# Kernel optimization log

Measured on AMD Instinct MI355X. Metric: run time of the kernel, lower is better.

## Reference

```python
import jax, jax.numpy as jnp
import numpy as np

B, S, D, H, E, K, V, FF, P = 1, 2048, 1024, 16, 8, 2, 32000, 4096, 4096
HD = D // H
EPS = 1e-5


def setup_inputs() -> dict:
    key = jax.random.key(0)
    ks = iter(jax.random.split(key, 64))
    w = lambda shape: jax.random.normal(next(ks), shape, jnp.float32) * 0.02
    d = {}
    d['input_ids'] = jax.random.randint(next(ks), (B, S), 0, V)
    d['embed_w'] = w((V, D))
    d['pos_w'] = w((P, D))
    for i in (0, 1):
        d[f'b{i}_ln1_g'] = jnp.ones(D); d[f'b{i}_ln1_b'] = jnp.zeros(D)
        d[f'b{i}_in_w'] = w((3 * D, D)); d[f'b{i}_in_b'] = jnp.zeros(3 * D)
        d[f'b{i}_out_w'] = w((D, D)); d[f'b{i}_out_b'] = jnp.zeros(D)
        d[f'b{i}_ln2_g'] = jnp.ones(D); d[f'b{i}_ln2_b'] = jnp.zeros(D)
    d['b0_ffn_w1'] = w((FF, D)); d['b0_ffn_b1'] = jnp.zeros(FF)
    d['b0_ffn_w2'] = w((D, FF)); d['b0_ffn_b2'] = jnp.zeros(D)
    d['b1_gate_w'] = w((E, D)); d['b1_gate_b'] = jnp.zeros(E)
    d['b1_moe_w1'] = w((E, FF, D)); d['b1_moe_b1'] = jnp.zeros((E, FF))
    d['b1_moe_w2'] = w((E, D, FF)); d['b1_moe_b2'] = jnp.zeros((E, D))
    d['norm_g'] = jnp.ones(D); d['norm_b'] = jnp.zeros(D)
    d['head_w'] = w((V, D))
    return d


def _ln(x, g, b):
    m = jnp.mean(x, -1, keepdims=True)
    v = jnp.mean(jnp.square(x - m), -1, keepdims=True)
    return (x - m) * jax.lax.rsqrt(v + EPS) * g + b


def _mha(x, in_w, in_b, out_w, out_b):
    # torch nn.MultiheadAttention (batch_first, eval mode -> no dropout)
    qkv = x @ in_w.T + in_b  # [B,S,3D]
    q, k, v = jnp.split(qkv, 3, axis=-1)
    q = q.reshape(B, S, H, HD); k = k.reshape(B, S, H, HD); v = v.reshape(B, S, H, HD)
    scores = jnp.einsum('bqhd,bkhd->bhqk', q, k) / jnp.sqrt(jnp.float32(HD))
    attn = jax.nn.softmax(scores, axis=-1)
    o = jnp.einsum('bhqk,bkhd->bqhd', attn, v).reshape(B, S, D)
    return o @ out_w.T + out_b


def _moe(h, gate_w, gate_b, w1, b1, w2, b2):
    scores = h @ gate_w.T + gate_b                       # [B,S,E]
    top_s, top_i = jax.lax.top_k(scores, K)              # [B,S,K]
    weights = jax.nn.softmax(top_s, axis=-1)             # softmax over top-k
    onehot = jax.nn.one_hot(top_i, E, dtype=h.dtype)     # [B,S,K,E]
    combine = jnp.sum(onehot * weights[..., None], axis=-2)  # [B,S,E]
    hid = jax.nn.gelu(jnp.einsum('bsd,efd->bsef', h, w1) + b1, approximate=False)
    eo = jnp.einsum('bsef,edf->bsed', hid, w2) + b2      # [B,S,E,D]
    return jnp.einsum('bsed,bse->bsd', eo, combine)


def reference(input_ids, embed_w, pos_w,
              b0_ln1_g, b0_ln1_b, b0_in_w, b0_in_b, b0_out_w, b0_out_b, b0_ln2_g, b0_ln2_b,
              b0_ffn_w1, b0_ffn_b1, b0_ffn_w2, b0_ffn_b2,
              b1_ln1_g, b1_ln1_b, b1_in_w, b1_in_b, b1_out_w, b1_out_b, b1_ln2_g, b1_ln2_b,
              b1_gate_w, b1_gate_b, b1_moe_w1, b1_moe_b1, b1_moe_w2, b1_moe_b2,
              norm_g, norm_b, head_w):
    pos = jnp.arange(S)[None, :]
    x = jnp.take(embed_w, input_ids, axis=0) + jnp.take(pos_w, pos, axis=0)
    # block 0: dense FFN
    x = x + _mha(_ln(x, b0_ln1_g, b0_ln1_b), b0_in_w, b0_in_b, b0_out_w, b0_out_b)
    h = _ln(x, b0_ln2_g, b0_ln2_b)
    ffn = jax.nn.gelu(h @ b0_ffn_w1.T + b0_ffn_b1, approximate=False) @ b0_ffn_w2.T + b0_ffn_b2
    x = x + ffn  # integration layer assumed residual add
    # block 1: MoE
    x = x + _mha(_ln(x, b1_ln1_g, b1_ln1_b), b1_in_w, b1_in_b, b1_out_w, b1_out_b)
    h = _ln(x, b1_ln2_g, b1_ln2_b)
    x = x + _moe(h, b1_gate_w, b1_gate_b, b1_moe_w1, b1_moe_b1, b1_moe_w2, b1_moe_b2)
    x = _ln(x, norm_g, norm_b)
    return x @ head_w.T
```

## Files before the change

### kernel.cpp

```cpp
#include <hip/hip_runtime.h>
#include <hip/hip_bf16.h>
#include <math.h>

typedef unsigned short ushort_t;
typedef __attribute__((ext_vector_type(8))) __bf16 bf16x8;
typedef __attribute__((ext_vector_type(4))) float f32x4;
typedef __attribute__((ext_vector_type(8))) short s8v;
typedef __attribute__((ext_vector_type(4))) short s4v;

#define SQ 2048
#define DM 1024
#define NH 16
#define HDIM 64
#define FFD 4096
#define NVOC 32000

__device__ inline float b2f(unsigned short u) {
  union { unsigned int i; float f; } x; x.i = ((unsigned int)u) << 16; return x.f;
}
__device__ inline unsigned short f2b(float f) {
  __hip_bfloat16 h = __float2bfloat16(f);
  return *reinterpret_cast<unsigned short*>(&h);
}
__device__ inline void split2(float x, ushort_t& h, ushort_t& l) {
  h = f2b(x);
  l = f2b(x - b2f(h));
}
__device__ inline float geluf(float v) {
  return 0.5f * v * (1.0f + erff(v * 0.70710678118654752f));
}
__device__ __forceinline__ void gld16(const void* g, void* l) {
  __builtin_amdgcn_global_load_lds(
      (const __attribute__((address_space(1))) void*)g,
      (__attribute__((address_space(3))) void*)l, 16, 0, 0);
}
#define MFMA __builtin_amdgcn_mfma_f32_16x16x32_bf16

template<int EPI, int NT, int KS>
__device__ __forceinline__ void gemmsp_body(
    const ushort_t* __restrict__ AH, const ushort_t* __restrict__ AL,
    int lda, long long bA,
    const ushort_t* __restrict__ BH, const ushort_t* __restrict__ BL,
    int ldb, long long bB,
    float* __restrict__ C, ushort_t* __restrict__ CH, ushort_t* __restrict__ CL,
    int ldc, long long bC, long long pC,
    int M, int N, int K, const float* __restrict__ bias, float alpha,
    ushort_t* __restrict__ TH, ushort_t* __restrict__ TL)
{
  int z = blockIdx.z, h = z / KS, kc = z % KS;
  const ushort_t* AHp = AH + (long long)h * bA + (long long)kc * K;
  const ushort_t* ALp = AL + (long long)h * bA + (long long)kc * K;
  const ushort_t* BHp = BH + (long long)h * bB + (long long)kc * K;
  const ushort_t* BLp = BL + (long long)h * bB + (long long)kc * K;
  int m0 = blockIdx.x * 128, n0 = blockIdx.y * NT;
  const int NF = NT / 32;

  __shared__ __align__(16) ushort_t sAH[128 * 32], sAL[128 * 32];
  __shared__ __align__(16) ushort_t sBH[NT * 32],  sBL[NT * 32];

  int tid = threadIdx.x, lane = tid & 63, wave = tid >> 6;
  int wr = (wave >> 1) * 64, wc = (wave & 1) * (NT >> 1);
  int l15 = lane & 15, l4 = lane >> 4;

  f32x4 acc[4][NF];
#pragma unroll
  for (int m = 0; m < 4; ++m)
#pragma unroll
    for (int n = 0; n < NF; ++n) acc[m][n] = (f32x4){0.f, 0.f, 0.f, 0.f};

  for (int k0 = 0; k0 < K; k0 += 32) {
#pragma unroll
    for (int i = 0; i < 2; ++i) {
      int fi = i * 2048 + tid * 8;
      int r = fi >> 5, chk = (fi >> 3) & 3;
      int scol = ((chk ^ ((r >> 1) & 3)) << 3);
      int ra = m0 + r; if (ra > M - 1) ra = M - 1;
      long long go = (long long)ra * lda + k0 + scol;
      gld16(AHp + go, &sAH[fi]);
      gld16(ALp + go, &sAL[fi]);
    }
#pragma unroll
    for (int i = 0; i < NT / 64; ++i) {
      int fi = i * 2048 + tid * 8;
      int r = fi >> 5, chk = (fi >> 3) & 3;
      int scol = ((chk ^ ((r >> 1) & 3)) << 3);
      int rb = n0 + r; if (rb > N - 1) rb = N - 1;
      long long go = (long long)rb * ldb + k0 + scol;
      gld16(BHp + go, &sBH[fi]);
      gld16(BLp + go, &sBL[fi]);
    }
    __syncthreads();
    bf16x8 ah[4], al[4], bh[NF], bl[NF];
#pragma unroll
    for (int m = 0; m < 4; ++m) {
      int r = wr + m * 16 + l15;
      int o = r * 32 + ((l4 ^ ((r >> 1) & 3)) << 3);
      ah[m] = *(const bf16x8*)&sAH[o];
      al[m] = *(const bf16x8*)&sAL[o];
    }
#pragma unroll
    for (int n = 0; n < NF; ++n) {
      int r = wc + n * 16 + l15;
      int o = r * 32 + ((l4 ^ ((r >> 1) & 3)) << 3);
      bh[n] = *(const bf16x8*)&sBH[o];
      bl[n] = *(const bf16x8*)&sBL[o];
    }
#pragma unroll
    for (int m = 0; m < 4; ++m)
#pragma unroll
      for (int n = 0; n < NF; ++n) {
        acc[m][n] = MFMA(ah[m], bh[n], acc[m][n], 0, 0, 0);
        acc[m][n] = MFMA(al[m], bh[n], acc[m][n], 0, 0, 0);
        acc[m][n] = MFMA(ah[m], bl[n], acc[m][n], 0, 0, 0);
      }
    __syncthreads();
  }

  if (EPI == 5 && n0 >= 2 * DM) {
#pragma unroll
    for (int m = 0; m < 4; ++m) {
      int rbase = m0 + wr + m * 16 + l4 * 4;
#pragma unroll
      for (int n = 0; n < NF; ++n) {
        int c = n0 + wc + n * 16 + l15;
        int d = c - 2 * DM;
        float bv = bias[c];
        s4v hv, lv;
#pragma unroll
        for (int q = 0; q < 4; ++q) {
          ushort_t hh, ll; split2(acc[m][n][q] + bv, hh, ll);
          hv[q] = (short)hh; lv[q] = (short)ll;
        }
        *(s4v*)&TH[(long long)d * SQ + rbase] = hv;
        *(s4v*)&TL[(long long)d * SQ + rbase] = lv;
      }
    }
    return;
  }

#pragma unroll
  for (int m = 0; m < 4; ++m) {
#pragma unroll
    for (int n = 0; n < NF; ++n) {
      int c = n0 + wc + n * 16 + l15;
      if (c >= N) continue;
      float bv = (EPI == 4 || EPI == 5) ? bias[c] : 0.f;
#pragma unroll
      for (int q = 0; q < 4; ++q) {
        int rr = m0 + wr + m * 16 + l4 * 4 + q;
        if (rr >= M) continue;
        float v = acc[m][n][q];
        if (EPI == 5) {
          ushort_t hh, ll; split2(v + bv, hh, ll);
          long long o = (long long)rr * ldc + c; CH[o] = hh; CL[o] = ll;
        } else if (EPI == 2) {
          C[(long long)kc * pC + (long long)rr * ldc + (long long)h * bC + c] = v;
        } else if (EPI == 4) {
          ushort_t hh, ll; split2(geluf(v + bv), hh, ll);
          long long o = (long long)rr * ldc + c; CH[o] = hh; CL[o] = ll;
        }
      }
    }
  }
}

#define SP_ARGS const ushort_t* AH, const ushort_t* AL, int lda, long long bA, \
    const ushort_t* BH, const ushort_t* BL, int ldb, long long bB, \
    float* C, ushort_t* CH, ushort_t* CL, int ldc, long long bC, long long pC, \
    int M, int N, int K, const float* bias, float alpha, \
    ushort_t* TH, ushort_t* TL
#define SP_PASS AH, AL, lda, bA, BH, BL, ldb, bB, C, CH, CL, ldc, bC, pC, M, N, K, bias, alpha, TH, TL

__global__ __launch_bounds__(256) void k_qkv (SP_ARGS) { gemmsp_body<5,128,1>(SP_PASS); }
__global__ __launch_bounds__(256) void k_outp(SP_ARGS) { gemmsp_body<2, 64,4>(SP_PASS); }
__global__ __launch_bounds__(256) void k_ffn1(SP_ARGS) { gemmsp_body<4,128,1>(SP_PASS); }
__global__ __launch_bounds__(256) void k_ffn2(SP_ARGS) { gemmsp_body<2, 64,2>(SP_PASS); }

__global__ __launch_bounds__(256)
void k_attn(const ushort_t* __restrict__ qkvH, const ushort_t* __restrict__ qkvL,
            const ushort_t* __restrict__ VtH, const ushort_t* __restrict__ VtL,
            ushort_t* __restrict__ aH, ushort_t* __restrict__ aL)
{
  int f = blockIdx.x + blockIdx.y * gridDim.x;
  int logical = (f & 7) * 64 + (f >> 3);
  int q0 = (logical & 31) * 64;
  int h  = logical >> 5;

  __shared__ __align__(16) ushort_t sKH[4096], sKL[4096];
  __shared__ __align__(16) ushort_t sVH[4096], sVL[4096];
  __shared__ __align__(16) ushort_t sPH[4096], sPL[4096];

  int tid = threadIdx.x, lane = tid & 63, wave = tid >> 6;
  int l15 = lane & 15, l4 = lane >> 4;

  bf16x8 qh[2], ql[2];
  {
    long long base = (long long)(q0 + wave * 16 + l15) * (3 * DM) + h * 64 + l4 * 8;
    qh[0] = *(const bf16x8*)(qkvH + base);
    qh[1] = *(const bf16x8*)(qkvH + base + 32);
    ql[0] = *(const bf16x8*)(qkvL + base);
    ql[1] = *(const bf16x8*)(qkvL + base + 32);
  }

  float mrow[4], lrow[4];
  f32x4 Oacc[4];
#pragma unroll
  for (int r = 0; r < 4; ++r) { mrow[r] = -1e30f; lrow[r] = 0.f; }
#pragma unroll
  for (int n = 0; n < 4; ++n) Oacc[n] = (f32x4){0.f, 0.f, 0.f, 0.f};

  for (int kt = 0; kt < SQ / 64; ++kt) {
#pragma unroll
    for (int i = 0; i < 2; ++i) {
      int idx = i * 2048 + tid * 8;
      int row = idx >> 6, chk = (idx >> 3) & 7;
      int scol = ((chk ^ (row & 7)) << 3);
      long long gk = (long long)(kt * 64 + row) * (3 * DM) + DM + h * 64 + scol;
      long long gv = (long long)(h * 64 + row) * SQ + kt * 64 + scol;
      gld16(qkvH + gk, &sKH[idx]);
      gld16(qkvL + gk, &sKL[idx]);
      gld16(VtH + gv, &sVH[idx]);
      gld16(VtL + gv, &sVL[idx]);
    }
    __syncthreads();

    f32x4 S[4];
#pragma unroll
    for (int n = 0; n < 4; ++n) S[n] = (f32x4){0.f, 0.f, 0.f, 0.f};
#pragma unroll
    for (int kk = 0; kk < 64; kk += 32) {
      int kkI = kk >> 5;
      bf16x8 qhf = qh[kkI], qlf = ql[kkI];
#pragma unroll
      for (int n = 0; n < 4; ++n) {
        int br = n * 16 + l15;
        int bo = br * 64 + ((((kk >> 3) + l4) ^ (br & 7)) << 3);
        bf16x8 kh = *(const bf16x8*)&sKH[bo];
        bf16x8 kl = *(const bf16x8*)&sKL[bo];
        S[n] = MFMA(qhf, kh, S[n], 0, 0, 0);
        S[n] = MFMA(qlf, kh, S[n], 0, 0, 0);
        S[n] = MFMA(qhf, kl, S[n], 0, 0, 0);
      }
    }
    float tm[4], ts[4];
#pragma unroll
    for (int r = 0; r < 4; ++r) {
#pragma unroll
      for (int n = 0; n < 4; ++n) S[n][r] *= 0.125f;
      tm[r] = fmaxf(fmaxf(S[0][r], S[1][r]), fmaxf(S[2][r], S[3][r]));
    }
#pragma unroll
    for (int mk = 1; mk <= 8; mk <<= 1)
#pragma unroll
      for (int r = 0; r < 4; ++r) tm[r] = fmaxf(tm[r], __shfl_xor(tm[r], mk));
#pragma unroll
    for (int r = 0; r < 4; ++r) {
      float mn = fmaxf(mrow[r], tm[r]);
      float corr = __expf(mrow[r] - mn);
      mrow[r] = mn;
      float s = 0.f;
#pragma unroll
      for (int n = 0; n < 4; ++n) { S[n][r] = __expf(S[n][r] - mn); s += S[n][r]; }
      ts[r] = s;
      lrow[r] *= corr;
#pragma unroll
      for (int n = 0; n < 4; ++n) Oacc[n][r] *= corr;
    }
#pragma unroll
    for (int mk = 1; mk <= 8; mk <<= 1)
#pragma unroll
      for (int r = 0; r < 4; ++r) ts[r] += __shfl_xor(ts[r], mk);
#pragma unroll
    for (int r = 0; r < 4; ++r) lrow[r] += ts[r];

    {
      ushort_t* pH = &sPH[wave * 1024];
      ushort_t* pL = &sPL[wave * 1024];
#pragma unroll
      for (int n = 0; n < 4; ++n)
#pragma unroll
        for (int r = 0; r < 4; ++r) {
          int row = l4 * 4 + r, col = n * 16 + l15;
          int ad = row * 64 + (((col >> 3) ^ (row & 7)) << 3) + (col & 7);
          ushort_t hh, ll; split2(S[n][r], hh, ll);
          pH[ad] = hh; pL[ad] = ll;
        }
    }
    __syncthreads();
#pragma unroll
    for (int kk = 0; kk < 64; kk += 32) {
      int ao = wave * 1024 + l15 * 64 + ((((kk >> 3) + l4) ^ (l15 & 7)) << 3);
      bf16x8 ph = *(const bf16x8*)&sPH[ao];
      bf16x8 pl = *(const bf16x8*)&sPL[ao];
#pragma unroll
      for (int n = 0; n < 4; ++n) {
        int br = n * 16 + l15;
        int bo = br * 64 + ((((kk >> 3) + l4) ^ (br & 7)) << 3);
        bf16x8 vh = *(const bf16x8*)&sVH[bo];
        bf16x8 vl = *(const bf16x8*)&sVL[bo];
        Oacc[n] = MFMA(ph, vh, Oacc[n], 0, 0, 0);
        Oacc[n] = MFMA(pl, vh, Oacc[n], 0, 0, 0);
        Oacc[n] = MFMA(ph, vl, Oacc[n], 0, 0, 0);
      }
    }
    __syncthreads();
  }

#pragma unroll
  for (int n = 0; n < 4; ++n)
#pragma unroll
    for (int r = 0; r < 4; ++r) {
      int q = q0 + wave * 16 + l4 * 4 + r;
      int d = h * 64 + n * 16 + l15;
      float val = Oacc[n][r] / lrow[r];
      ushort_t hh, ll; split2(val, hh, ll);
      long long o = (long long)q * DM + d;
      aH[o] = hh; aL[o] = ll;
    }
}

template<int EPI, int BSRC, int SWAP, int KS, int XS>
__device__ __forceinline__ void gemm16_body(
    const ushort_t* __restrict__ A, int lda, long long bA,
    const void* __restrict__ Bv, int ldb, long long bB,
    void* __restrict__ Cv, int ldc, long long bC, long long pC,
    int M, int N, int K, const float* __restrict__ bias, int bBias,
    const int* __restrict__ offs)
{
  int bz = blockIdx.z;
  int z = bz / KS, kc = bz % KS;
  int Kc = K / KS;
  const ushort_t* Ap = A + (long long)z * bA + (long long)kc * Kc;
  int rowStart = 0, Meff = M;
  if (offs) { rowStart = offs[z]; Meff = offs[z + 1] - rowStart; }
  int bx = blockIdx.x, by = blockIdx.y;
  if (XS) {
    int flat = bx + by * gridDim.x;
    int cpx = (gridDim.x * gridDim.y) >> 3;
    int s = (flat & 7) * cpx + (flat >> 3);
    bx = s % gridDim.x; by = s / gridDim.x;
  }
  int m0 = (SWAP ? by : bx) * 128;
  if (m0 >= Meff) return;
  int n0 = (SWAP ? bx : by) * 128;

  __shared__ __align__(16) char smem[32768];
  ushort_t* As = (ushort_t*)smem;
  ushort_t* Bs = (ushort_t*)(smem + 16384);

  int tid = threadIdx.x, lane = tid & 63, wave = tid >> 6;
  int wr = (wave >> 1) * 64, wc = (wave & 1) * 64;
  int l15 = lane & 15, l4 = lane >> 4;

  f32x4 acc[4][4];
#pragma unroll
  for (int m = 0; m < 4; ++m)
#pragma unroll
    for (int n = 0; n < 4; ++n) acc[m][n] = (f32x4){0.f, 0.f, 0.f, 0.f};

  for (int k0 = 0; k0 < Kc; k0 += 64) {
#pragma unroll
    for (int i = 0; i < 4; ++i) {
      int idx = i * 2048 + tid * 8;
      int row = idx >> 6, chk = (idx >> 3) & 7;
      int scol = ((chk ^ (row & 7)) << 3);
      int ra = m0 + row; if (ra > Meff - 1) ra = Meff - 1;
      gld16(Ap + (long long)(rowStart + ra) * lda + k0 + scol, &As[idx]);
    }
    if (BSRC == 1) {
      const ushort_t* Bp = (const ushort_t*)Bv + (long long)z * bB + (long long)kc * Kc;
#pragma unroll
      for (int i = 0; i < 4; ++i) {
        int idx = i * 2048 + tid * 8;
        int row = idx >> 6, chk = (idx >> 3) & 7;
        int scol = ((chk ^ (row & 7)) << 3);
        int rb = n0 + row; if (rb > N - 1) rb = N - 1;
        gld16(Bp + (long long)rb * ldb + k0 + scol, &Bs[idx]);
      }
    } else {
      const float* Bf = (const float*)Bv + (long long)z * bB + (long long)kc * Kc;
#pragma unroll
      for (int i = 0; i < 8; ++i) {
        int g = tid + i * 256;
        int r = g >> 4, c4 = (g & 15) * 4;
        int rb = n0 + r; if (rb > N - 1) rb = N - 1;
        float4 fv = *(const float4*)(Bf + (long long)rb * ldb + k0 + c4);
        s4v o; o[0] = (short)f2b(fv.x); o[1] = (short)f2b(fv.y);
        o[2] = (short)f2b(fv.z); o[3] = (short)f2b(fv.w);
        int dst = r * 64 + (((c4 >> 3) ^ (r & 7)) << 3) + (c4 & 7);
        *(s4v*)&Bs[dst] = o;
      }
    }
    __syncthreads();
#pragma unroll
    for (int kk = 0; kk < 64; kk += 32) {
      bf16x8 af[4], bfr[4];
#pragma unroll
      for (int m = 0; m < 4; ++m) {
        int r = wr + m * 16 + l15;
        af[m] = *(const bf16x8*)&As[r * 64 + ((((kk >> 3) + l4) ^ (r & 7)) << 3)];
      }
#pragma unroll
      for (int n = 0; n < 4; ++n) {
        int r = wc + n * 16 + l15;
        bfr[n] = *(const bf16x8*)&Bs[r * 64 + ((((kk >> 3) + l4) ^ (r & 7)) << 3)];
      }
#pragma unroll
      for (int m = 0; m < 4; ++m)
#pragma unroll
        for (int n = 0; n < 4; ++n)
          acc[m][n] = MFMA(af[m], bfr[n], acc[m][n], 0, 0, 0);
    }
    __syncthreads();
  }

  if (EPI == 6 || EPI == 7) {
    float* fE = (float*)smem;
#pragma unroll
    for (int h2 = 0; h2 < 2; ++h2) {
      if ((wave >> 1) == h2) {
#pragma unroll
        for (int m = 0; m < 4; ++m)
#pragma unroll
          for (int n = 0; n < 4; ++n)
#pragma unroll
            for (int q = 0; q < 4; ++q)
              fE[(m * 16 + l4 * 4 + q) * 128 + wc + n * 16 + l15] = acc[m][n][q];
      }
      __syncthreads();
#pragma unroll
      for (int i = 0; i < 8; ++i) {
        int lin = tid + i * 256;
        int row = lin >> 5, c4 = (lin & 31) << 2;
        int gr = m0 + h2 * 64 + row;
        if (gr < Meff) {
          f32x4 v4 = *(const f32x4*)&fE[row * 128 + c4];
          long long crow = rowStart + gr;
          float* dst = (float*)Cv + (EPI == 7 ? (long long)kc * pC : 0LL)
                       + crow * ldc + n0 + c4;
          if (EPI == 6) __builtin_nontemporal_store(v4, (f32x4*)dst);
          else          *(f32x4*)dst = v4;
        }
      }
      __syncthreads();
    }
    return;
  }

#pragma unroll
  for (int m = 0; m < 4; ++m) {
#pragma unroll
    for (int n = 0; n < 4; ++n) {
      int c = n0 + wc + n * 16 + l15;
      if (c >= N) continue;
      float bv = (EPI == 2) ? bias[(long long)z * bBias + c] : 0.f;
#pragma unroll
      for (int q = 0; q < 4; ++q) {
        int rr = m0 + wr + m * 16 + l4 * 4 + q;
        if (rr >= Meff) continue;
        float v = acc[m][n][q];
        long long crow = rowStart + rr;
        if (EPI == 2)
          ((ushort_t*)Cv)[crow * ldc + (long long)z * bC + c] = f2b(geluf(v + bv));
      }
    }
  }
}

#define G16_ARGS const ushort_t* A, int lda, long long bA, const void* Bv, \
    int ldb, long long bB, void* Cv, int ldc, long long bC, long long pC, \
    int M, int N, int K, const float* bias, int bBias, const int* offs
#define G16_PASS A, lda, bA, Bv, ldb, bB, Cv, ldc, bC, pC, M, N, K, bias, bBias, offs

__global__ __launch_bounds__(256) void k_moe1   (G16_ARGS) { gemm16_body<2,1,1,1,0>(G16_PASS); }
__global__ __launch_bounds__(256) void k_moe2   (G16_ARGS) { gemm16_body<7,1,1,2,0>(G16_PASS); }
__global__ __launch_bounds__(256) void k_head_bf(G16_ARGS) { gemm16_body<6,1,0,1,1>(G16_PASS); }
__global__ __launch_bounds__(256) void k_head_f (G16_ARGS) { gemm16_body<6,0,0,1,1>(G16_PASS); }

__global__ __launch_bounds__(256)
void cvt_split2(const float* __restrict__ s0, ushort_t* __restrict__ dh0,
                ushort_t* __restrict__ dl0,
                const float* __restrict__ s1, ushort_t* __restrict__ dh1,
                ushort_t* __restrict__ dl1, int n4)
{
  const float* s = blockIdx.y ? s1 : s0;
  ushort_t* dh = blockIdx.y ? dh1 : dh0;
  ushort_t* dl = blockIdx.y ? dl1 : dl0;
  int i = blockIdx.x * blockDim.x + threadIdx.x;
  int stride = gridDim.x * blockDim.x;
  for (; i < n4; i += stride) {
    float4 f = ((const float4*)s)[i];
    s4v h, l; ushort_t hh, ll;
    split2(f.x, hh, ll); h[0] = (short)hh; l[0] = (short)ll;
    split2(f.y, hh, ll); h[1] = (short)hh; l[1] = (short)ll;
    split2(f.z, hh, ll); h[2] = (short)hh; l[2] = (short)ll;
    split2(f.w, hh, ll); h[3] = (short)hh; l[3] = (short)ll;
    ((s4v*)dh)[i] = h; ((s4v*)dl)[i] = l;
  }
}

__global__ __launch_bounds__(256)
void cvt_bf16(const float* __restrict__ s, ushort_t* __restrict__ d, int n4)
{
  int i = blockIdx.x * blockDim.x + threadIdx.x;
  int stride = gridDim.x * blockDim.x;
  for (; i < n4; i += stride) {
    float4 f = ((const float4*)s)[i];
    s4v o; o[0] = (short)f2b(f.x); o[1] = (short)f2b(f.y);
    o[2] = (short)f2b(f.z); o[3] = (short)f2b(f.w);
    ((s4v*)d)[i] = o;
  }
}

__global__ __launch_bounds__(256)
void embed_kernel(const int* __restrict__ ids, const float* __restrict__ ew,
                  const float* __restrict__ pw, float* __restrict__ x,
                  int* __restrict__ counts)
{
  int srow = blockIdx.x, tid = threadIdx.x;
  if (srow == 0 && tid < 8) counts[tid] = 0;
  int id = ids[srow];
  const float4 e = *(const float4*)(ew + (long long)id * DM + tid * 4);
  const float4 p = *(const float4*)(pw + (long long)srow * DM + tid * 4);
  float4* xr = (float4*)(x + (long long)srow * DM) + tid;
  *xr = make_float4(e.x + p.x, e.y + p.y, e.z + p.z, e.w + p.w);
}

template<int MODE, int NP>
__global__ __launch_bounds__(256)
void ln_fused(float* __restrict__ x, const float* __restrict__ P, long long pC,
              const float* __restrict__ bias_pre,
              const float* __restrict__ g, const float* __restrict__ b,
              ushort_t* __restrict__ outH, ushort_t* __restrict__ outL)
{
  int row = blockIdx.x, tid = threadIdx.x;
  long long xo = (long long)row * DM + tid * 4;
  float4 v = *(const float4*)(x + xo);
  if (NP > 0) {
    float4 bp = *(const float4*)(bias_pre + tid * 4);
    float sx = bp.x, sy = bp.y, sz = bp.z, sw = bp.w;
#pragma unroll
    for (int p = 0; p < NP; ++p) {
      float4 pv = *(const float4*)(P + (long long)p * pC + xo);
      sx += pv.x; sy += pv.y; sz += pv.z; sw += pv.w;
    }
    v.x += sx; v.y += sy; v.z += sz; v.w += sw;
    *(float4*)(x + xo) = v;
  }
  __shared__ float sm1[4], sm2[4];
  float s = v.x + v.y + v.z + v.w;
  for (int o = 32; o > 0; o >>= 1) s += __shfl_down(s, o);
  if ((tid & 63) == 0) sm1[tid >> 6] = s;
  __syncthreads();
  float mean = (sm1[0] + sm1[1] + sm1[2] + sm1[3]) * (1.0f / DM);
  float d0 = v.x - mean, d1 = v.y - mean, d2 = v.z - mean, d3 = v.w - mean;
  float q = d0 * d0 + d1 * d1 + d2 * d2 + d3 * d3;
  for (int o = 32; o > 0; o >>= 1) q += __shfl_down(q, o);
  if ((tid & 63) == 0) sm2[tid >> 6] = q;
  __syncthreads();
  float var = (sm2[0] + sm2[1] + sm2[2] + sm2[3]) * (1.0f / DM);
  float rstd = rsqrtf(var + 1e-5f);
  float4 gv = ((const float4*)g)[tid];
  float4 bv = ((const float4*)b)[tid];
  float o0 = d0 * rstd * gv.x + bv.x, o1 = d1 * rstd * gv.y + bv.y;
  float o2 = d2 * rstd * gv.z + bv.z, o3 = d3 * rstd * gv.w + bv.w;
  long long base = (long long)row * DM + tid * 4;
  if (MODE == 0) {
    ushort_t hh, ll;
    split2(o0, hh, ll); outH[base + 0] = hh; outL[base + 0] = ll;
    split2(o1, hh, ll); outH[base + 1] = hh; outL[base + 1] = ll;
    split2(o2, hh, ll); outH[base + 2] = hh; outL[base + 2] = ll;
    split2(o3, hh, ll); outH[base + 3] = hh; outL[base + 3] = ll;
  } else {
    outH[base + 0] = f2b(o0); outH[base + 1] = f2b(o1);
    outH[base + 2] = f2b(o2); outH[base + 3] = f2b(o3);
  }
}

__global__ __launch_bounds__(256)
void ln_gate_top2(float* __restrict__ x, const float* __restrict__ P,
                  long long pC, const float* __restrict__ bias_pre,
                  const float* __restrict__ g, const float* __restrict__ b,
                  const float* __restrict__ gw, const float* __restrict__ gb,
                  int* __restrict__ topi, float* __restrict__ topw,
                  int* __restrict__ counts, ushort_t* __restrict__ outH)
{
  int row = blockIdx.x, tid = threadIdx.x;
  long long xo = (long long)row * DM + tid * 4;
  float4 v = *(const float4*)(x + xo);
  {
    float4 bp = *(const float4*)(bias_pre + tid * 4);
    float sx = bp.x, sy = bp.y, sz = bp.z, sw = bp.w;
#pragma unroll
    for (int p = 0; p < 4; ++p) {
      float4 pv = *(const float4*)(P + (long long)p * pC + xo);
      sx += pv.x; sy += pv.y; sz += pv.z; sw += pv.w;
    }
    v.x += sx; v.y += sy; v.z += sz; v.w += sw;
    *(float4*)(x + xo) = v;
  }
  __shared__ float sm1[4], sm2[4];
  __shared__ float se[8][4];
  float s = v.x + v.y + v.z + v.w;
  for (int o = 32; o > 0; o >>= 1) s += __shfl_down(s, o);
  if ((tid & 63) == 0) sm1[tid >> 6] = s;
  __syncthreads();
  float mean = (sm1[0] + sm1[1] + sm1[2] + sm1[3]) * (1.0f / DM);
  float d0 = v.x - mean, d1 = v.y - mean, d2 = v.z - mean, d3 = v.w - mean;
  float q = d0 * d0 + d1 * d1 + d2 * d2 + d3 * d3;
  for (int o = 32; o > 0; o >>= 1) q += __shfl_down(q, o);
  if ((tid & 63) == 0) sm2[tid >> 6] = q;
  __syncthreads();
  float var = (sm2[0] + sm2[1] + sm2[2] + sm2[3]) * (1.0f / DM);
  float rstd = rsqrtf(var + 1e-5f);
  float4 gv = ((const float4*)g)[tid];
  float4 bv = ((const float4*)b)[tid];
  float h0 = d0 * rstd * gv.x + bv.x, h1 = d1 * rstd * gv.y + bv.y;
  float h2 = d2 * rstd * gv.z + bv.z, h3 = d3 * rstd * gv.w + bv.w;
  long long base = (long long)row * DM + tid * 4;
  outH[base + 0] = f2b(h0); outH[base + 1] = f2b(h1);
  outH[base + 2] = f2b(h2); outH[base + 3] = f2b(h3);
#pragma unroll
  for (int e = 0; e < 8; ++e) {
    float4 w = ((const float4*)(gw + (long long)e * DM))[tid];
    float p = h0 * w.x + h1 * w.y + h2 * w.z + h3 * w.w;
    for (int o = 32; o > 0; o >>= 1) p += __shfl_down(p, o);
    if ((tid & 63) == 0) se[e][tid >> 6] = p;
  }
  __syncthreads();
  if (tid == 0) {
    float sc[8];
#pragma unroll
    for (int e = 0; e < 8; ++e)
      sc[e] = se[e][0] + se[e][1] + se[e][2] + se[e][3] + gb[e];
    int i1 = 0; float m1 = sc[0];
    for (int e = 1; e < 8; ++e) if (sc[e] > m1) { m1 = sc[e]; i1 = e; }
    int i2 = -1; float m2 = -1e30f;
    for (int e = 0; e < 8; ++e) if (e != i1 && sc[e] > m2) { m2 = sc[e]; i2 = e; }
    float e2 = __expf(m2 - m1);
    float w1 = 1.f / (1.f + e2);
    topi[row * 2] = i1; topi[row * 2 + 1] = i2;
    topw[row * 2] = w1; topw[row * 2 + 1] = 1.f - w1;
    atomicAdd(&counts[i1], 1);
    atomicAdd(&counts[i2], 1);
  }
}

__global__ void moe_prefix(const int* __restrict__ counts, int* __restrict__ offs,
                           int* __restrict__ cursors)
{
  if (threadIdx.x == 0 && blockIdx.x == 0) {
    int a = 0;
    for (int e = 0; e < 8; ++e) { offs[e] = a; a += counts[e]; cursors[e] = 0; }
    offs[8] = a;
  }
}

__global__ __launch_bounds__(256)
void moe_gather(const ushort_t* __restrict__ hH, const int* __restrict__ topi,
                const float* __restrict__ topw, const int* __restrict__ offs,
                int* __restrict__ cursors, int* __restrict__ tokIdx,
                float* __restrict__ tokW, int* __restrict__ slotOf,
                ushort_t* __restrict__ Xg)
{
  int tok = blockIdx.x, tid = threadIdx.x;
  __shared__ int s0s, s1s;
  if (tid == 0) {
    int e0 = topi[tok * 2], e1 = topi[tok * 2 + 1];
    int s0 = offs[e0] + atomicAdd(&cursors[e0], 1);
    int s1 = offs[e1] + atomicAdd(&cursors[e1], 1);
    tokIdx[s0] = tok; tokW[s0] = topw[tok * 2];
    tokIdx[s1] = tok; tokW[s1] = topw[tok * 2 + 1];
    slotOf[tok * 2] = s0; slotOf[tok * 2 + 1] = s1;
    s0s = s0; s1s = s1;
  }
  __syncthreads();
  s4v v = ((const s4v*)(hH + (long long)tok * DM))[tid];
  ((s4v*)(Xg + (long long)s0s * DM))[tid] = v;
  ((s4v*)(Xg + (long long)s1s * DM))[tid] = v;
}

__global__ __launch_bounds__(256)
void moe_ln_final(const float* __restrict__ x, const float* __restrict__ eo,
                  long long pC, const int* __restrict__ slotOf,
                  const int* __restrict__ topi, const float* __restrict__ topw,
                  const float* __restrict__ b2, const float* __restrict__ g,
                  const float* __restrict__ b, ushort_t* __restrict__ outH)
{
  int tok = blockIdx.x, tid = threadIdx.x;
  int s0 = slotOf[tok * 2], s1 = slotOf[tok * 2 + 1];
  int e0 = topi[tok * 2], e1 = topi[tok * 2 + 1];
  float w0 = topw[tok * 2], w1 = topw[tok * 2 + 1];
  float4 a  = ((const float4*)(eo + (long long)s0 * DM))[tid];
  float4 a2 = ((const float4*)(eo + pC + (long long)s0 * DM))[tid];
  float4 bb1= ((const float4*)(eo + (long long)s1 * DM))[tid];
  float4 bb2= ((const float4*)(eo + pC + (long long)s1 * DM))[tid];
  float4 ba = ((const float4*)(b2 + (long long)e0 * DM))[tid];
  float4 bbb= ((const float4*)(b2 + (long long)e1 * DM))[tid];
  float4 v = ((const float4*)(x + (long long)tok * DM))[tid];
  v.x += w0 * (a.x + a2.x + ba.x) + w1 * (bb1.x + bb2.x + bbb.x);
  v.y += w0 * (a.y + a2.y + ba.y) + w1 * (bb1.y + bb2.y + bbb.y);
  v.z += w0 * (a.z + a2.z + ba.z) + w1 * (bb1.z + bb2.z + bbb.z);
  v.w += w0 * (a.w + a2.w + ba.w) + w1 * (bb1.w + bb2.w + bbb.w);
  __shared__ float sm1[4], sm2[4];
  float s = v.x + v.y + v.z + v.w;
  for (int o = 32; o > 0; o >>= 1) s += __shfl_down(s, o);
  if ((tid & 63) == 0) sm1[tid >> 6] = s;
  __syncthreads();
  float mean = (sm1[0] + sm1[1] + sm1[2] + sm1[3]) * (1.0f / DM);
  float d0 = v.x - mean, d1 = v.y - mean, d2 = v.z - mean, d3 = v.w - mean;
  float q = d0 * d0 + d1 * d1 + d2 * d2 + d3 * d3;
  for (int o = 32; o > 0; o >>= 1) q += __shfl_down(q, o);
  if ((tid & 63) == 0) sm2[tid >> 6] = q;
  __syncthreads();
  float var = (sm2[0] + sm2[1] + sm2[2] + sm2[3]) * (1.0f / DM);
  float rstd = rsqrtf(var + 1e-5f);
  float4 gv = ((const float4*)g)[tid];
  float4 bv = ((const float4*)b)[tid];
  long long base = (long long)tok * DM + tid * 4;
  outH[base + 0] = f2b(d0 * rstd * gv.x + bv.x);
  outH[base + 1] = f2b(d1 * rstd * gv.y + bv.y);
  outH[base + 2] = f2b(d2 * rstd * gv.z + bv.z);
  outH[base + 3] = f2b(d3 * rstd * gv.w + bv.w);
}

extern "C" void kernel_launch(void* const* d_in, const int* in_sizes, int n_in,
                              void* d_out, int out_size, void* d_ws, size_t ws_size,
                              hipStream_t stream)
{
  const int* ids = (const int*)d_in[0];
  const float* embed_w = (const float*)d_in[1];
  const float* pos_w   = (const float*)d_in[2];
  const float* ln1_g[2] = {(const float*)d_in[3],  (const float*)d_in[11]};
  const float* ln1_b[2] = {(const float*)d_in[4],  (const float*)d_in[12]};
  const float* in_w[2]  = {(const float*)d_in[5],  (const float*)d_in[13]};
  const float* in_b[2]  = {(const float*)d_in[6],  (const float*)d_in[14]};
  const float* out_w[2] = {(const float*)d_in[7],  (const float*)d_in[15]};
  const float* out_b[2] = {(const float*)d_in[8],  (const float*)d_in[16]};
  const float* ln2_g[2] = {(const float*)d_in[9],  (const float*)d_in[17]};
  const float* ln2_b[2] = {(const float*)d_in[10], (const float*)d_in[18]};
  const float* ffn_w1 = (const float*)d_in[19];
  const float* ffn_b1 = (const float*)d_in[20];
  const float* ffn_w2 = (const float*)d_in[21];
  const float* ffn_b2 = (const float*)d_in[22];
  const float* gate_w = (const float*)d_in[23];
  const float* gate_b = (const float*)d_in[24];
  const float* moe_w1 = (const float*)d_in[25];
  const float* moe_b1 = (const float*)d_in[26];
  const float* moe_w2 = (const float*)d_in[27];
  const float* moe_b2 = (const float*)d_in[28];
  const float* norm_g = (const float*)d_in[29];
  const float* norm_b = (const float*)d_in[30];
  const float* head_w = (const float*)d_in[31];

  char* ob = (char*)d_out;
  size_t off = 0;
  auto alloc = [&](size_t bytes) {
    char* p = ob + off;
    off = (off + bytes + 255) & ~(size_t)255;
    return p;
  };
  float*    x      = (float*)alloc((size_t)SQ * DM * 4);
  ushort_t* hbufH  = (ushort_t*)alloc((size_t)SQ * DM * 2);
  ushort_t* hbufL  = (ushort_t*)alloc((size_t)SQ * DM * 2);
  ushort_t* qkvH   = (ushort_t*)alloc((size_t)SQ * 3 * DM * 2);
  ushort_t* qkvL   = (ushort_t*)alloc((size_t)SQ * 3 * DM * 2);
  ushort_t* VtH    = (ushort_t*)alloc((size_t)NH * HDIM * SQ * 2);
  ushort_t* VtL    = (ushort_t*)alloc((size_t)NH * HDIM * SQ * 2);
  char*     resv   = (char*)alloc((size_t)32 << 20);
  ushort_t* attnH  = (ushort_t*)alloc((size_t)SQ * DM * 2);
  ushort_t* attnL  = (ushort_t*)alloc((size_t)SQ * DM * 2);
  ushort_t* Xg     = (ushort_t*)alloc((size_t)2 * SQ * DM * 2);
  int*      topi   = (int*)alloc(SQ * 2 * 4);
  float*    topw   = (float*)alloc(SQ * 2 * 4);
  int*      tokIdx = (int*)alloc(2 * SQ * 4);
  float*    tokW   = (float*)alloc(2 * SQ * 4);
  int*      slotOf = (int*)alloc(2 * SQ * 4);
  int*      counts = (int*)alloc(256);
  int*      offsb  = (int*)alloc(256);
  int*      cursors= (int*)alloc(256);
  ushort_t* ffnH   = (ushort_t*)alloc((size_t)SQ * FFD * 2);
  ushort_t* ffnL   = (ushort_t*)alloc((size_t)SQ * FFD * 2);
  float*    eo     = (float*)alloc((size_t)2 * 2 * SQ * DM * 4);
  ushort_t* inwH[2], *inwL[2], *outwH[2], *outwL[2];
  ushort_t* wsplit0 = (ushort_t*)alloc(0);
  inwH[0]  = (ushort_t*)alloc((size_t)3 * DM * DM * 2);
  inwL[0]  = (ushort_t*)alloc((size_t)3 * DM * DM * 2);
  inwH[1]  = (ushort_t*)alloc((size_t)3 * DM * DM * 2);
  inwL[1]  = (ushort_t*)alloc((size_t)3 * DM * DM * 2);
  outwH[0] = (ushort_t*)alloc((size_t)DM * DM * 2);
  outwL[0] = (ushort_t*)alloc((size_t)DM * DM * 2);
  outwH[1] = (ushort_t*)alloc((size_t)DM * DM * 2);
  outwL[1] = (ushort_t*)alloc((size_t)DM * DM * 2);
  ushort_t* f1H = (ushort_t*)alloc((size_t)FFD * DM * 2);
  ushort_t* f1L = (ushort_t*)alloc((size_t)FFD * DM * 2);
  ushort_t* f2H = (ushort_t*)alloc((size_t)DM * FFD * 2);
  ushort_t* f2L = (ushort_t*)alloc((size_t)DM * FFD * 2);
  ushort_t* moe_w1b = wsplit0;
  ushort_t* moe_w2b = qkvH;
  ushort_t* moehid  = ffnH;
  float*    pp      = eo;
  const long long eoPC = (long long)2 * SQ * DM;
  const long long ppPC = (long long)SQ * DM;
  ushort_t* hfin    = (ushort_t*)d_ws;
  bool wsBig = ws_size >= ((size_t)70 << 20);
  ushort_t* head_wb = (ushort_t*)((char*)d_ws + ((size_t)4 << 20));
  (void)resv;

  embed_kernel<<<SQ, 256, 0, stream>>>(ids, embed_w, pos_w, x, counts);
  cvt_split2<<<dim3(512, 2), 256, 0, stream>>>(
      in_w[0], inwH[0], inwL[0], in_w[1], inwH[1], inwL[1], 3 * DM * DM / 4);
  cvt_split2<<<dim3(512, 2), 256, 0, stream>>>(
      out_w[0], outwH[0], outwL[0], out_w[1], outwH[1], outwL[1], DM * DM / 4);
  cvt_split2<<<dim3(512, 2), 256, 0, stream>>>(
      ffn_w1, f1H, f1L, ffn_w2, f2H, f2L, FFD * DM / 4);
  if (wsBig)
    cvt_bf16<<<1024, 256, 0, stream>>>(head_w, head_wb, NVOC * DM / 4);

  ln_fused<0, 0><<<SQ, 256, 0, stream>>>(x, nullptr, 0, nullptr,
                                         ln1_g[0], ln1_b[0], hbufH, hbufL);
  k_qkv<<<dim3(16, 24, 1), 256, 0, stream>>>(
      hbufH, hbufL, DM, 0, inwH[0], inwL[0], DM, 0,
      nullptr, qkvH, qkvL, 3 * DM, 0, 0,
      SQ, 3 * DM, DM, in_b[0], 1.f, VtH, VtL);
  k_attn<<<dim3(SQ / 64, NH), 256, 0, stream>>>(qkvH, qkvL, VtH, VtL,
                                                attnH, attnL);
  k_outp<<<dim3(16, 16, 4), 256, 0, stream>>>(
      attnH, attnL, DM, 0, outwH[0], outwL[0], DM, 0,
      pp, nullptr, nullptr, DM, 0, ppPC,
      SQ, DM, DM / 4, nullptr, 1.f, nullptr, nullptr);
  ln_fused<0, 4><<<SQ, 256, 0, stream>>>(x, pp, ppPC, out_b[0],
                                         ln2_g[0], ln2_b[0], hbufH, hbufL);
  k_ffn1<<<dim3(16, 32, 1), 256, 0, stream>>>(
      hbufH, hbufL, DM, 0, f1H, f1L, DM, 0,
      nullptr, ffnH, ffnL, FFD, 0, 0,
      SQ, FFD, DM, ffn_b1, 1.f, nullptr, nullptr);
  k_ffn2<<<dim3(16, 16, 2), 256, 0, stream>>>(
      ffnH, ffnL, FFD, 0, f2H, f2L, FFD, 0,
      pp, nullptr, nullptr, DM, 0, ppPC,
      SQ, DM, FFD / 2, nullptr, 1.f, nullptr, nullptr);
  ln_fused<0, 2><<<SQ, 256, 0, stream>>>(x, pp, ppPC, ffn_b2,
                                         ln1_g[1], ln1_b[1], hbufH, hbufL);
  k_qkv<<<dim3(16, 24, 1), 256, 0, stream>>>(
      hbufH, hbufL, DM, 0, inwH[1], inwL[1], DM, 0,
      nullptr, qkvH, qkvL, 3 * DM, 0, 0,
      SQ, 3 * DM, DM, in_b[1], 1.f, VtH, VtL);
  k_attn<<<dim3(SQ / 64, NH), 256, 0, stream>>>(qkvH, qkvL, VtH, VtL,
                                                attnH, attnL);
  k_outp<<<dim3(16, 16, 4), 256, 0, stream>>>(
      attnH, attnL, DM, 0, outwH[1], outwL[1], DM, 0,
      pp, nullptr, nullptr, DM, 0, ppPC,
      SQ, DM, DM / 4, nullptr, 1.f, nullptr, nullptr);
  cvt_bf16<<<2048, 256, 0, stream>>>(moe_w1, moe_w1b, 8 * FFD * DM / 4);
  cvt_bf16<<<2048, 256, 0, stream>>>(moe_w2, moe_w2b, 8 * DM * FFD / 4);
  ln_gate_top2<<<SQ, 256, 0, stream>>>(x, pp, ppPC, out_b[1],
                                       ln2_g[1], ln2_b[1], gate_w, gate_b,
                                       topi, topw, counts, hbufH);
  moe_prefix<<<1, 64, 0, stream>>>(counts, offsb, cursors);
  moe_gather<<<SQ, 256, 0, stream>>>(hbufH, topi, topw, offsb, cursors,
                                     tokIdx, tokW, slotOf, Xg);
  k_moe1<<<dim3(32, 16, 8), 256, 0, stream>>>(
      Xg, DM, 0, moe_w1b, DM, (long long)FFD * DM,
      moehid, FFD, 0, 0, SQ, FFD, DM, moe_b1, FFD, offsb);
  k_moe2<<<dim3(8, 16, 16), 256, 0, stream>>>(
      moehid, FFD, 0, moe_w2b, FFD, (long long)DM * FFD,
      eo, DM, 0, eoPC, SQ, DM, FFD, nullptr, 0, offsb);
  moe_ln_final<<<SQ, 256, 0, stream>>>(x, eo, eoPC, slotOf, topi, topw,
                                       moe_b2, norm_g, norm_b, hfin);
  if (wsBig)
    k_head_bf<<<dim3(16, 250, 1), 256, 0, stream>>>(
        hfin, DM, 0, head_wb, DM, 0, d_out, NVOC, 0, 0,
        SQ, NVOC, DM, nullptr, 0, nullptr);
  else
    k_head_f<<<dim3(16, 250, 1), 256, 0, stream>>>(
        hfin, DM, 0, head_w, DM, 0, d_out, NVOC, 0, 0,
        SQ, NVOC, DM, nullptr, 0, nullptr);
}
```

Baseline: 1.216 ms.

## Double-buffer GEMM shared-memory tiles and merge MoE weight conversion launches

The generic bf16 GEMM kernel now keeps two shared-memory stages (64KB total) and issues the global loads for the next K-tile before running MFMAs on the current one. This drops one barrier per iteration and lets load latency overlap compute. The price is double the LDS per block, which can cut how many blocks fit on a CU. Separately, the two MoE weight fp32-to-bf16 conversion kernels become a single launch with a 2D grid.

```diff
diff --git a/kernel.cpp b/kernel.cpp
--- a/kernel.cpp
+++ b/kernel.cpp
@@ -344,9 +344,11 @@
   if (m0 >= Meff) return;
   int n0 = (SWAP ? bx : by) * 128;
 
-  __shared__ __align__(16) char smem[32768];
-  ushort_t* As = (ushort_t*)smem;
-  ushort_t* Bs = (ushort_t*)(smem + 16384);
+  __shared__ __align__(16) char smem[65536];
+  const ushort_t* Bp = (BSRC == 1)
+      ? (const ushort_t*)Bv + (long long)z * bB + (long long)kc * Kc : nullptr;
+  const float* Bf = (BSRC == 0)
+      ? (const float*)Bv + (long long)z * bB + (long long)kc * Kc : nullptr;
 
   int tid = threadIdx.x, lane = tid & 63, wave = tid >> 6;
   int wr = (wave >> 1) * 64, wc = (wave & 1) * 64;
@@ -358,27 +360,27 @@
 #pragma unroll
     for (int n = 0; n < 4; ++n) acc[m][n] = (f32x4){0.f, 0.f, 0.f, 0.f};
 
-  for (int k0 = 0; k0 < Kc; k0 += 64) {
+  auto stageG = [&](int buf, int k0) {
+    ushort_t* dA = (ushort_t*)smem + buf * 8192;
+    ushort_t* dB = (ushort_t*)smem + 16384 + buf * 8192;
 #pragma unroll
     for (int i = 0; i < 4; ++i) {
       int idx = i * 2048 + tid * 8;
       int row = idx >> 6, chk = (idx >> 3) & 7;
       int scol = ((chk ^ (row & 7)) << 3);
       int ra = m0 + row; if (ra > Meff - 1) ra = Meff - 1;
-      gld16(Ap + (long long)(rowStart + ra) * lda + k0 + scol, &As[idx]);
+      gld16(Ap + (long long)(rowStart + ra) * lda + k0 + scol, &dA[idx]);
     }
     if (BSRC == 1) {
-      const ushort_t* Bp = (const ushort_t*)Bv + (long long)z * bB + (long long)kc * Kc;
 #pragma unroll
       for (int i = 0; i < 4; ++i) {
         int idx = i * 2048 + tid * 8;
         int row = idx >> 6, chk = (idx >> 3) & 7;
         int scol = ((chk ^ (row & 7)) << 3);
         int rb = n0 + row; if (rb > N - 1) rb = N - 1;
-        gld16(Bp + (long long)rb * ldb + k0 + scol, &Bs[idx]);
+        gld16(Bp + (long long)rb * ldb + k0 + scol, &dB[idx]);
       }
     } else {
-      const float* Bf = (const float*)Bv + (long long)z * bB + (long long)kc * Kc;
 #pragma unroll
       for (int i = 0; i < 8; ++i) {
         int g = tid + i * 256;
@@ -388,10 +390,19 @@
         s4v o; o[0] = (short)f2b(fv.x); o[1] = (short)f2b(fv.y);
         o[2] = (short)f2b(fv.z); o[3] = (short)f2b(fv.w);
         int dst = r * 64 + (((c4 >> 3) ^ (r & 7)) << 3) + (c4 & 7);
-        *(s4v*)&Bs[dst] = o;
-      }
-    }
+        *(s4v*)&dB[dst] = o;
+      }
+    }
+  };
+
+  int nIt = Kc >> 6;
+  stageG(0, 0);
+  for (int it = 0; it < nIt; ++it) {
+    int cur = it & 1;
     __syncthreads();
+    if (it + 1 < nIt) stageG(cur ^ 1, (it + 1) << 6);
+    ushort_t* As = (ushort_t*)smem + cur * 8192;
+    ushort_t* Bs = (ushort_t*)smem + 16384 + cur * 8192;
 #pragma unroll
     for (int kk = 0; kk < 64; kk += 32) {
       bf16x8 af[4], bfr[4];
@@ -411,8 +422,8 @@
         for (int n = 0; n < 4; ++n)
           acc[m][n] = MFMA(af[m], bfr[n], acc[m][n], 0, 0, 0);
     }
-    __syncthreads();
-  }
+  }
+  __syncthreads();
 
   if (EPI == 6 || EPI == 7) {
     float* fE = (float*)smem;
@@ -502,6 +513,22 @@
 __global__ __launch_bounds__(256)
 void cvt_bf16(const float* __restrict__ s, ushort_t* __restrict__ d, int n4)
 {
+  int i = blockIdx.x * blockDim.x + threadIdx.x;
+  int stride = gridDim.x * blockDim.x;
+  for (; i < n4; i += stride) {
+    float4 f = ((const float4*)s)[i];
+    s4v o; o[0] = (short)f2b(f.x); o[1] = (short)f2b(f.y);
+    o[2] = (short)f2b(f.z); o[3] = (short)f2b(f.w);
+    ((s4v*)d)[i] = o;
+  }
+}
+
+__global__ __launch_bounds__(256)
+void cvt_bf16_2(const float* __restrict__ s0, ushort_t* __restrict__ d0,
+                const float* __restrict__ s1, ushort_t* __restrict__ d1, int n4)
+{
+  const float* s = blockIdx.y ? s1 : s0;
+  ushort_t* d = blockIdx.y ? d1 : d0;
   int i = blockIdx.x * blockDim.x + threadIdx.x;
   int stride = gridDim.x * blockDim.x;
   for (; i < n4; i += stride) {
@@ -851,8 +878,8 @@
       attnH, attnL, DM, 0, outwH[1], outwL[1], DM, 0,
       pp, nullptr, nullptr, DM, 0, ppPC,
       SQ, DM, DM / 4, nullptr, 1.f, nullptr, nullptr);
-  cvt_bf16<<<2048, 256, 0, stream>>>(moe_w1, moe_w1b, 8 * FFD * DM / 4);
-  cvt_bf16<<<2048, 256, 0, stream>>>(moe_w2, moe_w2b, 8 * DM * FFD / 4);
+  cvt_bf16_2<<<dim3(2048, 2), 256, 0, stream>>>(
+      moe_w1, moe_w1b, moe_w2, moe_w2b, 8 * FFD * DM / 4);
   ln_gate_top2<<<SQ, 256, 0, stream>>>(x, pp, ppPC, out_b[1],
                                        ln2_g[1], ln2_b[1], gate_w, gate_b,
                                        topi, topw, counts, hbufH);
```

After: 1.159 ms. 1.05x faster.
